# Optimization experiments

Measured on AMD Instinct MI355X. Metric: run time of the kernel, lower is better.

The kernel has to match this reference:

```python
import jax, jax.numpy as jnp
import numpy as np

INV_SQRT3 = 0.5773502691896258  # e3nn wigner_3j entries for (0,1,1),(1,0,1),(1,1,0)


def setup_inputs() -> dict:
    key = jax.random.key(0)
    ks = jax.random.split(key, 9)
    B, N = 2, 256
    d_in, m1 = 256, 1          # input irreps: d_in x0e + m1 x1o
    d_h, m5, m3 = 256, 5, 3    # hidden irreps: d_h x0e + 5 x1o + 3 x1o
    d_out = 2                  # output irreps: 2 x0e
    return {
        "vectors": jax.random.normal(ks[0], (B, N, 3 * m1), jnp.float32),
        "scalars": jax.random.normal(ks[1], (B, N, d_in), jnp.float32),
        # e3nn internal weights ~ N(0,1); one weight block per CG path (uvw)
        "W1": jax.random.normal(ks[2], (d_in, d_in, d_h), jnp.float32),   # 0e x 0e -> 0e
        "W2a": jax.random.normal(ks[3], (d_in, m1, m5), jnp.float32),     # 0e x 1o -> 1o (mul 5)
        "W2b": jax.random.normal(ks[4], (d_in, m1, m3), jnp.float32),     # 0e x 1o -> 1o (mul 3)
        "W3a": jax.random.normal(ks[5], (m1, d_in, m5), jnp.float32),     # 1o x 0e -> 1o (mul 5)
        "W3b": jax.random.normal(ks[6], (m1, d_in, m3), jnp.float32),     # 1o x 0e -> 1o (mul 3)
        "W4": jax.random.normal(ks[7], (m1, m1, d_h), jnp.float32),       # 1o x 1o -> 0e
        "WL": jax.random.normal(ks[8], (d_h, d_out), jnp.float32),        # Linear d_h x0e -> 2 x0e
    }


def reference(vectors, scalars, W1, W2a, W2b, W3a, W3b, W4, WL):
    B, N, d = scalars.shape
    m1 = vectors.shape[-1] // 3
    z = B * N
    s = scalars.reshape(z, d)          # (z, d)  scalar (0e) channels
    v = vectors.reshape(z, m1, 3)      # (z, m1, 3)  vector (1o) channels
    d_h = W1.shape[-1]
    # e3nn FullyConnectedTensorProduct path weights ('component' irrep norm,
    # 'element' path norm): sqrt(ir_out.dim / sum_paths(mul1*mul2))
    pw0 = (1.0 / (d * d + m1 * m1)) ** 0.5      # into 0e output (paths 0e*0e and 1o*1o)
    pw1 = (3.0 / (2.0 * d * m1)) ** 0.5         # into each 1o output (paths 0e*1o and 1o*0e)
    # --- 0e x 0e -> 0e (dominant path) + 1o x 1o -> 0e ---
    t = jnp.einsum('zu,uvw->zvw', s, W1)        # (z, d, d_h)
    out0 = jnp.einsum('zv,zvw->zw', s, t)       # (z, d_h)
    out0 = out0 + INV_SQRT3 * jnp.einsum('zui,zvi,uvw->zw', v, v, W4)
    out0 = pw0 * out0
    # --- 0e x 1o -> 1o and 1o x 0e -> 1o (present in hidden irreps; they have
    # no path into the final 2x0e output, kept for structural fidelity) ---
    out1 = pw1 * INV_SQRT3 * (jnp.einsum('zu,zvk,uvw->zwk', s, v, W2a)
                              + jnp.einsum('zuk,zv,uvw->zwk', v, s, W3a))  # (z,5,3)
    out2 = pw1 * INV_SQRT3 * (jnp.einsum('zu,zvk,uvw->zwk', s, v, W2b)
                              + jnp.einsum('zuk,zv,uvw->zwk', v, s, W3b))  # (z,3,3)
    del out1, out2
    # --- e3nn Linear(hidden, 2x0e): only 0e->0e path, 1/sqrt(fan_in) norm ---
    lin = jnp.einsum('zu,uw->zw', out0, WL) / (d_h ** 0.5)   # (z, 2)
    m_eqv = lin[:, :1].reshape(B, N, 1)
    m_inv = lin[:, 1:].reshape(B, N, 1)
    return (m_eqv, m_inv)
```

## Files before the change

### kernel.cpp

```cpp
#include <hip/hip_runtime.h>


typedef __attribute__((ext_vector_type(8))) _Float16 f16x8;
typedef __attribute__((ext_vector_type(2))) _Float16 f16x2;
typedef __attribute__((ext_vector_type(4))) float f32x4;
typedef __attribute__((ext_vector_type(2))) int int2v;
typedef __attribute__((ext_vector_type(4))) int int4v;

#define LDS_S 16384
#define BP 80
#define BSTEP 5120
#define LDS_TOTAL (LDS_S + 4 * BSTEP)

__device__ __forceinline__ unsigned pkrtz(float a, float b) {
  return __builtin_bit_cast(unsigned, __builtin_amdgcn_cvt_pkrtz(a, b));
}
__device__ __forceinline__ int hbits(f16x2 h) {
  return __builtin_bit_cast(int, h);
}
__device__ __forceinline__ void barrier_lds() {
  asm volatile("s_waitcnt lgkmcnt(0)" ::: "memory");
  __builtin_amdgcn_s_barrier();
}

__global__ __launch_bounds__(256, 4) void eg_gemm(const float* __restrict__ s,
                                                  const float* __restrict__ W1,
                                                  float* __restrict__ out0) {
  extern __shared__ char smem[];
  char* sB = smem + LDS_S;

  const int bx = blockIdx.x;
  const int zh = bx >> 8;
  const int uvw = bx & 255;
  const int wt = uvw & 3, vc = (uvw >> 2) & 7, uc = uvw >> 5;
  const int u0 = uc * 32, v0 = vc * 32, w0 = wt * 64;

  const int t = threadIdx.x;
  const int lane = t & 63;
  const int wid = t >> 6;
  const int l15 = lane & 15;
  const int g = lane >> 4;

  for (int j = 0; j < 8; ++j) {
    int id = j * 256 + t;
    int zl = id >> 4;
    int c4 = id & 15;
    int srccol = (c4 < 8) ? (u0 + (c4 << 2)) : (v0 + ((c4 - 8) << 2));
    const float4 f = *(const float4*)(s + (zh * 128 + zl) * 256 + srccol);
    int slot = c4 >> 1;
    char* dst = smem + zl * 128 + (((slot ^ (zl & 7)) << 4) | ((c4 & 1) << 3));
    *(int2v*)dst = int2v{(int)pkrtz(f.x, f.y), (int)pkrtz(f.z, f.w)};
  }

  const int wB = t & 63;
  const int vg = t >> 6;
  const int hsw = (wB >> 3) & 7;
  const int sl0 = (vg ^ hsw) << 3;
  const int sl1 = ((vg + 4) ^ hsw) << 3;
  const float* gB = W1 + (size_t)u0 * 65536 + (v0 + vg * 4) * 256 + w0 + wB;

  float pf0[16], pf1[16];

#define ISSUE_TO(dst, usbase)                                               \
  do {                                                                      \
    const float* q0_ = gB + (size_t)(usbase) * 65536;                       \
    dst[0] = q0_[0];          dst[1] = q0_[256];                            \
    dst[2] = q0_[512];        dst[3] = q0_[768];                            \
    dst[4] = q0_[4096];       dst[5] = q0_[4096 + 256];                     \
    dst[6] = q0_[4096 + 512]; dst[7] = q0_[4096 + 768];                     \
    const float* q1_ = q0_ + 65536;                                         \
    dst[8] = q1_[0];           dst[9] = q1_[256];                           \
    dst[10] = q1_[512];        dst[11] = q1_[768];                          \
    dst[12] = q1_[4096];       dst[13] = q1_[4096 + 256];                   \
    dst[14] = q1_[4096 + 512]; dst[15] = q1_[4096 + 768];                   \
  } while (0)

#define WRITE_FROM(src, dst0_)                                              \
  do {                                                                      \
    char* d0_ = (dst0_);                                                    \
    *(int2v*)(d0_ + wB * BP + sl0) =                                        \
        int2v{(int)pkrtz(src[0], src[1]), (int)pkrtz(src[2], src[3])};      \
    *(int2v*)(d0_ + wB * BP + sl1) =                                        \
        int2v{(int)pkrtz(src[4], src[5]), (int)pkrtz(src[6], src[7])};      \
    char* d1_ = d0_ + BSTEP;                                                \
    *(int2v*)(d1_ + wB * BP + sl0) =                                        \
        int2v{(int)pkrtz(src[8], src[9]), (int)pkrtz(src[10], src[11])};    \
    *(int2v*)(d1_ + wB * BP + sl1) =                                        \
        int2v{(int)pkrtz(src[12], src[13]), (int)pkrtz(src[14], src[15])};  \
  } while (0)

  ISSUE_TO(pf0, 0);
  WRITE_FROM(pf0, sB);
  ISSUE_TO(pf0, 2);
  ISSUE_TO(pf1, 4);
  barrier_lds();

  const int swz = l15 & 7;
  int4v sv[2];
#pragma unroll
  for (int mf = 0; mf < 2; ++mf) {
    const char* p = smem + (wid * 32 + mf * 16 + l15) * 128 + (((4 + g) ^ swz) << 4);
    sv[mf] = *(const int4v*)p;
  }

  int baddr[4];
#pragma unroll
  for (int nf = 0; nf < 4; ++nf) {
    int w = nf * 16 + l15;
    baddr[nf] = w * BP + (((2 * g) ^ ((w >> 3) & 7)) << 3);
  }

  f32x4 acc[2][4];
#pragma unroll
  for (int a = 0; a < 2; ++a)
#pragma unroll
    for (int b = 0; b < 4; ++b) acc[a][b] = 0.f;

  for (int q = 0; q < 8; ++q) {
    int2v sur[2];
#pragma unroll
    for (int mf = 0; mf < 2; ++mf) {
      const char* p = smem + (wid * 32 + mf * 16 + l15) * 128 +
                      ((((q >> 1) ^ swz) << 4) | ((q & 1) << 3));
      sur[mf] = *(const int2v*)p;
    }
#pragma unroll
    for (int rr = 0; rr < 2; ++rr) {
      const int r = 2 * q + rr;
      const char* bufc = sB + rr * (2 * BSTEP);
      char* bufn = sB + (rr ^ 1) * (2 * BSTEP);
#pragma unroll
      for (int p = 0; p < 2; ++p) {
        f16x8 afr[2];
#pragma unroll
        for (int mf = 0; mf < 2; ++mf) {
          unsigned dw = (unsigned)sur[mf][rr];
          unsigned s2 = __builtin_amdgcn_perm(dw, dw, p ? 0x03020302u : 0x01000100u);
          f16x2 su2 = __builtin_bit_cast(f16x2, s2);
          int4v af;
#pragma unroll
          for (int jj = 0; jj < 4; ++jj) {
            f16x2 pv = __builtin_bit_cast(f16x2, (unsigned)sv[mf][jj]);
            f16x2 pr = su2 * pv;
            af[jj] = hbits(pr);
          }
          afr[mf] = __builtin_bit_cast(f16x8, af);
        }
        const char* bp = bufc + p * BSTEP;
#pragma unroll
        for (int nf = 0; nf < 4; ++nf) {
          int2v d0 = *(const int2v*)(bp + baddr[nf]);
          int2v d1 = *(const int2v*)(bp + (baddr[nf] ^ 8));
          int4v bf4 = int4v{d0[0], d0[1], d1[0], d1[1]};
          f16x8 bfr = __builtin_bit_cast(f16x8, bf4);
#pragma unroll
          for (int mf = 0; mf < 2; ++mf)
            acc[mf][nf] =
                __builtin_amdgcn_mfma_f32_16x16x32_f16(afr[mf], bfr, acc[mf][nf], 0, 0, 0);
        }
      }
      if (r < 15) {
        if (rr == 0) WRITE_FROM(pf0, bufn); else WRITE_FROM(pf1, bufn);
      }
      if (r <= 12) {
        if (rr == 0) ISSUE_TO(pf0, 2 * (r + 3)); else ISSUE_TO(pf1, 2 * (r + 3));
      }
      if (r < 15) barrier_lds();
    }
  }

  const int rot = (uc ^ vc) & 3;
#pragma unroll
  for (int mf = 0; mf < 2; ++mf)
#pragma unroll
    for (int nf = 0; nf < 4; ++nf) {
      const int nfr = (nf + rot) & 3;
#pragma unroll
      for (int rI = 0; rI < 4; ++rI) {
        int z = zh * 128 + wid * 32 + mf * 16 + g * 4 + rI;
        int w = w0 + nfr * 16 + l15;
        atomicAdd(out0 + z * 256 + w, acc[mf][nfr][rI]);
      }
    }
}

__global__ void eg_finish(const float* __restrict__ vec,
                          const float* __restrict__ W4,
                          const float* __restrict__ WL,
                          const float* __restrict__ acc,
                          float* __restrict__ out) {
  const int z = blockIdx.x;
  const int lane = threadIdx.x;
  float v0 = vec[z * 3 + 0], v1 = vec[z * 3 + 1], v2 = vec[z * 3 + 2];
  const float b = 0.57735026918962576f * (v0 * v0 + v1 * v1 + v2 * v2);
  float a0 = 0.f, a1 = 0.f;
#pragma unroll
  for (int j = 0; j < 4; ++j) {
    int w = j * 64 + lane;
    float o = acc[z * 256 + w] + b * W4[w];
    a0 += o * WL[2 * w];
    a1 += o * WL[2 * w + 1];
  }
#pragma unroll
  for (int off = 32; off > 0; off >>= 1) {
    a0 += __shfl_xor(a0, off);
    a1 += __shfl_xor(a1, off);
  }
  if (lane == 0) {
    out[z] = 2.4413876e-04f * a0;
    out[512 + z] = 2.4413876e-04f * a1;
  }
}

extern "C" void kernel_launch(void* const* d_in, const int* in_sizes, int n_in,
                              void* d_out, int out_size, void* d_ws, size_t ws_size,
                              hipStream_t stream) {
  const float* vectors = (const float*)d_in[0];
  const float* scalars = (const float*)d_in[1];
  const float* W1 = (const float*)d_in[2];
  const float* W4 = (const float*)d_in[7];
  const float* WL = (const float*)d_in[8];
  float* out = (float*)d_out;
  float* acc = (float*)d_ws;

  (void)hipMemsetAsync(acc, 0, 512 * 256 * sizeof(float), stream);
  eg_gemm<<<1024, 256, LDS_TOTAL, stream>>>(scalars, W1, acc);
  eg_finish<<<512, 64, 0, stream>>>(vectors, W4, WL, acc, out);
}
```

Before: 177.9 us.

## Fuse final linear projection into GEMM epilogue to shrink atomic output

```diff
diff --git a/kernel.cpp b/kernel.cpp
--- a/kernel.cpp
+++ b/kernel.cpp
@@ -25,7 +25,8 @@
 
 __global__ __launch_bounds__(256, 4) void eg_gemm(const float* __restrict__ s,
                                                   const float* __restrict__ W1,
-                                                  float* __restrict__ out0) {
+                                                  const float* __restrict__ WL,
+                                                  float* __restrict__ oacc) {
   extern __shared__ char smem[];
   char* sB = smem + LDS_S;
 
@@ -169,17 +170,32 @@
     }
   }
 
-  const int rot = (uc ^ vc) & 3;
+  float2 wl[4];
+#pragma unroll
+  for (int nf = 0; nf < 4; ++nf) {
+    int w = w0 + nf * 16 + l15;
+    wl[nf] = *(const float2*)(WL + 2 * w);
+  }
 #pragma unroll
   for (int mf = 0; mf < 2; ++mf)
 #pragma unroll
-    for (int nf = 0; nf < 4; ++nf) {
-      const int nfr = (nf + rot) & 3;
-#pragma unroll
-      for (int rI = 0; rI < 4; ++rI) {
+    for (int rI = 0; rI < 4; ++rI) {
+      float s0 = 0.f, s1 = 0.f;
+#pragma unroll
+      for (int nf = 0; nf < 4; ++nf) {
+        float v = acc[mf][nf][rI];
+        s0 += v * wl[nf].x;
+        s1 += v * wl[nf].y;
+      }
+#pragma unroll
+      for (int off = 8; off > 0; off >>= 1) {
+        s0 += __shfl_xor(s0, off);
+        s1 += __shfl_xor(s1, off);
+      }
+      if (l15 == 0) {
         int z = zh * 128 + wid * 32 + mf * 16 + g * 4 + rI;
-        int w = w0 + nfr * 16 + l15;
-        atomicAdd(out0 + z * 256 + w, acc[mf][nfr][rI]);
+        atomicAdd(oacc + 2 * z, s0);
+        atomicAdd(oacc + 2 * z + 1, s1);
       }
     }
 }
@@ -187,7 +203,7 @@
 __global__ void eg_finish(const float* __restrict__ vec,
                           const float* __restrict__ W4,
                           const float* __restrict__ WL,
-                          const float* __restrict__ acc,
+                          const float* __restrict__ oacc,
                           float* __restrict__ out) {
   const int z = blockIdx.x;
   const int lane = threadIdx.x;
@@ -197,9 +213,10 @@
 #pragma unroll
   for (int j = 0; j < 4; ++j) {
     int w = j * 64 + lane;
-    float o = acc[z * 256 + w] + b * W4[w];
-    a0 += o * WL[2 * w];
-    a1 += o * WL[2 * w + 1];
+    float w4 = W4[w];
+    float2 l = *(const float2*)(WL + 2 * w);
+    a0 += w4 * l.x;
+    a1 += w4 * l.y;
   }
 #pragma unroll
   for (int off = 32; off > 0; off >>= 1) {
@@ -207,8 +224,8 @@
     a1 += __shfl_xor(a1, off);
   }
   if (lane == 0) {
-    out[z] = 2.4413876e-04f * a0;
-    out[512 + z] = 2.4413876e-04f * a1;
+    out[z] = 2.4413876e-04f * (oacc[2 * z] + b * a0);
+    out[512 + z] = 2.4413876e-04f * (oacc[2 * z + 1] + b * a1);
   }
 }
 
@@ -221,9 +238,9 @@
   const float* W4 = (const float*)d_in[7];
   const float* WL = (const float*)d_in[8];
   float* out = (float*)d_out;
-  float* acc = (float*)d_ws;
-
-  (void)hipMemsetAsync(acc, 0, 512 * 256 * sizeof(float), stream);
-  eg_gemm<<<1024, 256, LDS_TOTAL, stream>>>(scalars, W1, acc);
-  eg_finish<<<512, 64, 0, stream>>>(vectors, W4, WL, acc, out);
-}
+  float* oacc = (float*)d_ws;
+
+  (void)hipMemsetAsync(oacc, 0, 512 * 2 * sizeof(float), stream);
+  eg_gemm<<<1024, 256, LDS_TOTAL, stream>>>(scalars, W1, WL, oacc);
+  eg_finish<<<512, 64, 0, stream>>>(vectors, W4, WL, oacc, out);
+}
```

Measured after the change: 211.6 us. 19.0% more time.
